# Kernel tuning notes

Measured on AMD Instinct MI355X. Metric: run time of the kernel, lower is better.

Reference implementation:

```python
import jax, jax.numpy as jnp
import numpy as np

N = 100000      # nodes
E = 1200000     # edges
D_IN = 128      # input_dim
H = 64          # hidden_dim
OUT = 3         # output_dim
EPS = 1e-5      # BatchNorm eps


def setup_inputs() -> dict:
    key = jax.random.key(0)
    ks = jax.random.split(key, 24)
    w = lambda k, shape: jax.random.normal(k, shape, jnp.float32) * 0.05
    return {
        "x": jax.random.normal(ks[0], (N, D_IN), jnp.float32),
        "edge_index": jax.random.randint(ks[1], (2, E), 0, N, dtype=jnp.int32),
        "proj_W": w(ks[2], (H, D_IN)), "proj_b": w(ks[3], (H,)),
        "conv1_W": w(ks[4], (H, H)), "conv1_b": w(ks[5], (H,)),
        "bn1_g": jnp.ones((H,), jnp.float32), "bn1_b": w(ks[6], (H,)),
        "conv2_W": w(ks[7], (H, H)), "conv2_b": w(ks[8], (H,)),
        "bn2_g": jnp.ones((H,), jnp.float32), "bn2_b": w(ks[9], (H,)),
        "conv3_W": w(ks[10], (H, H)), "conv3_b": w(ks[11], (H,)),
        "bn3_g": jnp.ones((H,), jnp.float32), "bn3_b": w(ks[12], (H,)),
        "byp_W": w(ks[13], (OUT, D_IN)), "byp_b": w(ks[14], (OUT,)),
        "head_W": w(ks[15], (OUT, H + OUT)), "head_b": w(ks[16], (OUT,)),
    }


def reference(x, edge_index, proj_W, proj_b,
              conv1_W, conv1_b, bn1_g, bn1_b,
              conv2_W, conv2_b, bn2_g, bn2_b,
              conv3_W, conv3_b, bn3_g, bn3_b,
              byp_W, byp_b, head_W, head_b):
    n = x.shape[0]
    row, col = edge_index[0], edge_index[1]
    loop = jnp.arange(n, dtype=row.dtype)
    row_f = jnp.concatenate([row, loop])   # source (with self loops)
    col_f = jnp.concatenate([col, loop])   # target
    # symmetric GCN normalization: deg over targets of A+I, edge weight 1
    deg = jax.ops.segment_sum(jnp.ones(row_f.shape, jnp.float32), col_f, num_segments=n)
    dinv = jnp.where(deg > 0, jax.lax.rsqrt(deg), 0.0)
    norm = dinv[row_f] * dinv[col_f]       # [E+N]

    def gcn(h, W, b):
        h = h @ W.T                                    # transform then propagate
        msg = h[row_f] * norm[:, None]                 # gather + scale
        return jax.ops.segment_sum(msg, col_f, num_segments=n) + b

    def bn(h, g, b):
        # eval-mode BatchNorm1d: running_mean=0, running_var=1 buffers
        return h * (g / jnp.sqrt(1.0 + EPS)) + b

    h = x @ proj_W.T + proj_b
    idn = h
    h = jax.nn.relu(bn(gcn(h, conv1_W, conv1_b), bn1_g, bn1_b)) + idn  # dropout inactive (eval)
    idn = h
    h = jax.nn.relu(bn(gcn(h, conv2_W, conv2_b), bn2_g, bn2_b)) + idn
    h = jax.nn.relu(bn(gcn(h, conv3_W, conv3_b), bn3_g, bn3_b))

    byp = x @ byp_W.T + byp_b
    p = jnp.concatenate([h, byp], axis=1) @ head_W.T + head_b
    kappa = jnp.clip(p[:, 0] * 5.0 + 2.5, 0.2, 10.0)
    alpha = p[:, 1]
    tau = jnp.clip(p[:, 2] + 0.5, 0.05, 2.0)
    return jnp.stack([kappa, alpha, tau], axis=1)
```

## Files before the change

kernel.cpp:

```cpp
#include <hip/hip_runtime.h>
#include <hip/hip_fp16.h>

#define NN 100000
#define NE 1200000
#define NBUK ((NN + 127) / 128)
#define NCHUNK 512
#define NPROJ ((NN + 63) / 64)

typedef _Float16 h8 __attribute__((ext_vector_type(8)));
typedef float f32x4 __attribute__((ext_vector_type(4)));
typedef float f32x2 __attribute__((ext_vector_type(2)));

__global__ __launch_bounds__(256) void k_fusedA(const int* __restrict__ col,
                                                int* __restrict__ blkcnt,
                                                const float* __restrict__ X,
                                                const float* __restrict__ projW,
                                                const float* __restrict__ projb,
                                                const float* __restrict__ bypW,
                                                const float* __restrict__ bypb,
                                                _Float16* __restrict__ Yh,
                                                float* __restrict__ bypOut) {
    constexpr int D = 128, RS = D + 8, KS = D / 32;
    __shared__ _Float16 Xh[64 * RS];
    __shared__ _Float16 Wh[64 * RS];
    const int tid = threadIdx.x;

    if (blockIdx.x < NCHUNK) {
        int* lh = (int*)Xh;
        const int per = (NE + NCHUNK - 1) / NCHUNK;
        const int e0 = blockIdx.x * per;
        const int e1 = (e0 + per < NE) ? (e0 + per) : NE;
        for (int i = tid; i < NBUK; i += 256) lh[i] = 0;
        __syncthreads();
        for (int e = e0 + tid; e < e1; e += 256)
            atomicAdd(&lh[col[e] >> 7], 1);
        __syncthreads();
        for (int b = tid; b < NBUK; b += 256)
            blkcnt[b * NCHUNK + blockIdx.x] = lh[b];
        return;
    }

    const int n0 = (blockIdx.x - NCHUNK) * 64;

    for (int i = tid; i < 64 * (D / 8); i += 256) {
        int j = i / (D / 8), d8 = (i % (D / 8)) * 8;
        const float4* wp = (const float4*)&projW[j * D + d8];
        float4 w0 = wp[0], w1 = wp[1];
        h8 h = { (_Float16)w0.x, (_Float16)w0.y, (_Float16)w0.z, (_Float16)w0.w,
                 (_Float16)w1.x, (_Float16)w1.y, (_Float16)w1.z, (_Float16)w1.w };
        *(h8*)&Wh[j * RS + d8] = h;
    }
    for (int i = tid; i < 64 * (D / 8); i += 256) {
        int nl = i / (D / 8), d8 = (i % (D / 8)) * 8;
        int n = n0 + nl; if (n >= NN) n = NN - 1;
        const float4* xp = (const float4*)&X[(size_t)n * D + d8];
        float4 x0 = xp[0], x1 = xp[1];
        h8 h = { (_Float16)x0.x, (_Float16)x0.y, (_Float16)x0.z, (_Float16)x0.w,
                 (_Float16)x1.x, (_Float16)x1.y, (_Float16)x1.z, (_Float16)x1.w };
        *(h8*)&Xh[nl * RS + d8] = h;
    }
    __syncthreads();

    const int wid = tid >> 6, lane = tid & 63;
    const int lm = lane & 15, lq = lane >> 4;
    const int mBase = wid * 16;

    h8 bfrag[4][KS];
    #pragma unroll
    for (int t = 0; t < 4; ++t)
        #pragma unroll
        for (int s = 0; s < KS; ++s)
            bfrag[t][s] = *(const h8*)&Wh[(t * 16 + lm) * RS + s * 32 + lq * 8];

    h8 bfragB[KS];
    #pragma unroll
    for (int s = 0; s < KS; ++s) {
        if (lm < 3) {
            const float4* wp = (const float4*)&bypW[lm * D + s * 32 + lq * 8];
            float4 w0 = wp[0], w1 = wp[1];
            bfragB[s] = (h8){ (_Float16)w0.x, (_Float16)w0.y, (_Float16)w0.z, (_Float16)w0.w,
                              (_Float16)w1.x, (_Float16)w1.y, (_Float16)w1.z, (_Float16)w1.w };
        } else {
            bfragB[s] = (h8)(_Float16)0;
        }
    }

    f32x4 acc[5] = {};
    #pragma unroll
    for (int s = 0; s < KS; ++s) {
        h8 a = *(const h8*)&Xh[(mBase + lm) * RS + s * 32 + lq * 8];
        #pragma unroll
        for (int t = 0; t < 4; ++t)
            acc[t] = __builtin_amdgcn_mfma_f32_16x16x32_f16(a, bfrag[t][s], acc[t], 0, 0, 0);
        acc[4] = __builtin_amdgcn_mfma_f32_16x16x32_f16(a, bfragB[s], acc[4], 0, 0, 0);
    }

    float bb[4];
    #pragma unroll
    for (int t = 0; t < 4; ++t) bb[t] = projb[t * 16 + lm];
    float bypbv = (lm < 3) ? bypb[lm] : 0.f;
    const int nodeBase = n0 + mBase + lq * 4;

    #pragma unroll
    for (int r = 0; r < 4; ++r) {
        int node = nodeBase + r;
        if (node < NN) {
            #pragma unroll
            for (int t = 0; t < 4; ++t)
                Yh[(size_t)node * 64 + t * 16 + lm] = (_Float16)(acc[t][r] + bb[t]);
            if (lm < 3)
                bypOut[node * 3 + lm] = acc[4][r] + bypbv;
        }
    }
}

__global__ __launch_bounds__(1024) void k_scanAll(int* __restrict__ blkcnt,
                                                  int* __restrict__ bcnt) {
    __shared__ int s[1024];
    const int b = blockIdx.x, tid = threadIdx.x;
    int v = (tid < NCHUNK) ? blkcnt[b * NCHUNK + tid] : 0;
    s[tid] = v;
    __syncthreads();
    #pragma unroll
    for (int d = 1; d < 1024; d <<= 1) {
        int t = (tid >= d) ? s[tid - d] : 0;
        __syncthreads();
        s[tid] += t;
        __syncthreads();
    }
    if (tid < NCHUNK) blkcnt[b * NCHUNK + tid] = s[tid] - v;
    if (tid == 1023) bcnt[b] = s[1023];
}

__global__ __launch_bounds__(256) void k_bucketB(const int* __restrict__ row,
                                                 const int* __restrict__ col,
                                                 const int* __restrict__ bcnt,
                                                 const int* __restrict__ blkcnt,
                                                 unsigned* __restrict__ tmp) {
    __shared__ int lh[NBUK];
    __shared__ int part[256];
    const int tid = threadIdx.x;
    int loc[4]; int sum = 0;
    #pragma unroll
    for (int j = 0; j < 4; ++j) {
        int idx = tid * 4 + j;
        loc[j] = sum;
        sum += (idx < NBUK) ? bcnt[idx] : 0;
    }
    part[tid] = sum;
    __syncthreads();
    #pragma unroll
    for (int d = 1; d < 256; d <<= 1) {
        int t = (tid >= d) ? part[tid - d] : 0;
        __syncthreads();
        part[tid] += t;
        __syncthreads();
    }
    const int excl = part[tid] - sum;
    #pragma unroll
    for (int j = 0; j < 4; ++j) {
        int idx = tid * 4 + j;
        if (idx < NBUK)
            lh[idx] = excl + loc[j] + blkcnt[idx * NCHUNK + blockIdx.x];
    }
    __syncthreads();
    const int per = (NE + NCHUNK - 1) / NCHUNK;
    const int e0 = blockIdx.x * per;
    const int e1 = (e0 + per < NE) ? (e0 + per) : NE;
    for (int e = e0 + tid; e < e1; e += 256) {
        int c = col[e], r = row[e];
        int pos = atomicAdd(&lh[c >> 7], 1);
        tmp[pos] = ((unsigned)r << 7) | (unsigned)(c & 127);
    }
}

__global__ __launch_bounds__(256) void k_buildM(const unsigned* __restrict__ tmp,
                                                const int* __restrict__ bcnt,
                                                int* __restrict__ off,
                                                float* __restrict__ dinv,
                                                int* __restrict__ csr_row,
                                                const _Float16* __restrict__ hA,
                                                const float* __restrict__ W1,
                                                unsigned char* __restrict__ Y8) {
    constexpr int RS2 = 72;
    __shared__ int cnt[128], s[128], cur[128];
    __shared__ int red[256];
    __shared__ float dinvL[128];
    __shared__ _Float16 Hs[128 * RS2];
    __shared__ _Float16 WsL[64 * RS2];
    const int b = blockIdx.x, tid = threadIdx.x;

    for (int i = tid; i < 128 * 8; i += 256) {
        int j = i >> 3, d8 = (i & 7) * 8;
        int n = (b << 7) + j; if (n >= NN) n = NN - 1;
        *(h8*)&Hs[j * RS2 + d8] = *(const h8*)&hA[(size_t)n * 64 + d8];
    }
    for (int i = tid; i < 64 * 8; i += 256) {
        int j = i >> 3, d8 = (i & 7) * 8;
        const float4* wp = (const float4*)&W1[j * 64 + d8];
        float4 w0 = wp[0], w1 = wp[1];
        h8 h = { (_Float16)w0.x, (_Float16)w0.y, (_Float16)w0.z, (_Float16)w0.w,
                 (_Float16)w1.x, (_Float16)w1.y, (_Float16)w1.z, (_Float16)w1.w };
        *(h8*)&WsL[j * RS2 + d8] = h;
    }

    int ssum = 0;
    for (int i = tid; i < b; i += 256) ssum += bcnt[i];
    red[tid] = ssum;
    __syncthreads();
    #pragma unroll
    for (int d = 128; d > 0; d >>= 1) {
        if (tid < d) red[tid] += red[tid + d];
        __syncthreads();
    }
    const int seg0 = red[0];
    const int seg1 = seg0 + bcnt[b];
    const int colBase = b << 7;
    const int nCols = (NN - colBase < 128) ? (NN - colBase) : 128;
    if (tid < 128) cnt[tid] = 0;
    __syncthreads();
    for (int i = seg0 + tid; i < seg1; i += 256)
        atomicAdd(&cnt[tmp[i] & 127], 1);
    __syncthreads();
    if (tid < 128) s[tid] = cnt[tid];
    __syncthreads();
    #pragma unroll
    for (int d = 1; d < 128; d <<= 1) {
        int t = (tid < 128 && tid >= d) ? s[tid - d] : 0;
        __syncthreads();
        if (tid < 128) s[tid] += t;
        __syncthreads();
    }
    if (tid < 128) {
        float dv = rsqrtf((float)cnt[tid] + 1.0f);
        dinvL[tid] = dv;
        if (tid < nCols) {
            int exc = seg0 + s[tid] - cnt[tid];
            off[colBase + tid] = exc;
            cur[tid] = exc;
            dinv[colBase + tid] = dv;
        }
    }
    if (b == 0 && tid == 0) off[NN] = NE;
    __syncthreads();
    for (int i = seg0 + tid; i < seg1; i += 256) {
        unsigned v = tmp[i];
        int pos = atomicAdd(&cur[v & 127u], 1);
        csr_row[pos] = (int)(v >> 7);
    }
    __syncthreads();

    const int wid = tid >> 6, lane = tid & 63;
    const int lm = lane & 15, lq = lane >> 4;
    const int mBase = wid * 16;
    h8 cfrag[4][2];
    #pragma unroll
    for (int t = 0; t < 4; ++t)
        #pragma unroll
        for (int sx = 0; sx < 2; ++sx)
            cfrag[t][sx] = *(const h8*)&WsL[(t * 16 + lm) * RS2 + sx * 32 + lq * 8];
    #pragma unroll
    for (int hh = 0; hh < 2; ++hh) {
        const int rb = hh * 64 + mBase;
        f32x4 acc2[4] = {};
        #pragma unroll
        for (int sx = 0; sx < 2; ++sx) {
            h8 a = *(const h8*)&Hs[(rb + lm) * RS2 + sx * 32 + lq * 8];
            #pragma unroll
            for (int t = 0; t < 4; ++t)
                acc2[t] = __builtin_amdgcn_mfma_f32_16x16x32_f16(a, cfrag[t][sx], acc2[t], 0, 0, 0);
        }
        #pragma unroll
        for (int r = 0; r < 4; ++r) {
            int nl = rb + lq * 4 + r;
            int node = colBase + nl;
            if (node < NN) {
                float sdv = dinvL[nl];
                #pragma unroll
                for (int t = 0; t < 4; ++t) {
                    float v = acc2[t][r] * sdv;
                    int pk = __builtin_amdgcn_cvt_pk_fp8_f32(v, v, 0, false);
                    Y8[(size_t)node * 64 + t * 16 + lm] = (unsigned char)(pk & 0xff);
                }
            }
        }
    }
}

template<bool HEAD>
__global__ __launch_bounds__(256) void k_gather(const unsigned char* __restrict__ hB8,
                                                const float* __restrict__ dinv,
                                                const int* __restrict__ off,
                                                const int* __restrict__ csr_row,
                                                const float* __restrict__ convb,
                                                const float* __restrict__ bng,
                                                const float* __restrict__ bnb,
                                                _Float16* __restrict__ hA,
                                                const float* __restrict__ nextW,
                                                unsigned char* __restrict__ Y8,
                                                const float* __restrict__ byp,
                                                const float* __restrict__ headW,
                                                const float* __restrict__ headb,
                                                float* __restrict__ out) {
    constexpr int RS2 = 72;
    __shared__ _Float16 Ws[HEAD ? 1 : 64 * RS2];
    __shared__ _Float16 Hs[HEAD ? 1 : 32 * RS2];
    __shared__ float HWs[HEAD ? 204 : 1];
    const int tid = threadIdx.x;
    if constexpr (HEAD) {
        for (int i = tid; i < 204; i += 256)
            HWs[i] = (i < 201) ? headW[i] : headb[i - 201];
        __syncthreads();
    } else {
        for (int i = tid; i < 64 * 8; i += 256) {
            int j = i >> 3, d8 = (i & 7) * 8;
            const float4* wp = (const float4*)&nextW[j * 64 + d8];
            float4 w0 = wp[0], w1 = wp[1];
            h8 h = { (_Float16)w0.x, (_Float16)w0.y, (_Float16)w0.z, (_Float16)w0.w,
                     (_Float16)w1.x, (_Float16)w1.y, (_Float16)w1.z, (_Float16)w1.w };
            *(h8*)&Ws[j * RS2 + d8] = h;
        }
    }
    const int wid = tid >> 6, lane = tid & 63;
    const int nloc = wid * 8 + (lane >> 3);
    const int n = blockIdx.x * 32 + nloc;
    const int oct = lane & 7;
    const int f0 = oct * 8;

    const int e0 = off[n];
    const int deg = off[n + 1] - e0;
    int m = deg;
    #pragma unroll
    for (int mask = 8; mask < 64; mask <<= 1) {
        int o = __shfl_xor(m, mask, 64);
        m = (o > m) ? o : m;
    }

    const uint2* rows8 = (const uint2*)hB8;
    float acc[8] = {0, 0, 0, 0, 0, 0, 0, 0};
    uint2 selfw = rows8[(size_t)n * 8 + oct];
    {
        f32x2 p0 = __builtin_amdgcn_cvt_pk_f32_fp8(selfw.x, false);
        f32x2 p1 = __builtin_amdgcn_cvt_pk_f32_fp8(selfw.x, true);
        f32x2 p2 = __builtin_amdgcn_cvt_pk_f32_fp8(selfw.y, false);
        f32x2 p3 = __builtin_amdgcn_cvt_pk_f32_fp8(selfw.y, true);
        acc[0] += p0.x; acc[1] += p0.y; acc[2] += p1.x; acc[3] += p1.y;
        acc[4] += p2.x; acc[5] += p2.y; acc[6] += p3.x; acc[7] += p3.y;
    }
    for (int it = 0; it < m; it += 8) {
        uint2 w[8];
        #pragma unroll
        for (int q = 0; q < 8; ++q) {
            bool vq = it + q < deg;
            int rq = csr_row[vq ? e0 + it + q : 0];
            w[q] = rows8[(size_t)rq * 8 + oct];
            if (!vq) { w[q].x = 0; w[q].y = 0; }
        }
        #pragma unroll
        for (int q = 0; q < 8; ++q) {
            f32x2 p0 = __builtin_amdgcn_cvt_pk_f32_fp8(w[q].x, false);
            f32x2 p1 = __builtin_amdgcn_cvt_pk_f32_fp8(w[q].x, true);
            f32x2 p2 = __builtin_amdgcn_cvt_pk_f32_fp8(w[q].y, false);
            f32x2 p3 = __builtin_amdgcn_cvt_pk_f32_fp8(w[q].y, true);
            acc[0] += p0.x; acc[1] += p0.y; acc[2] += p1.x; acc[3] += p1.y;
            acc[4] += p2.x; acc[5] += p2.y; acc[6] += p3.x; acc[7] += p3.y;
        }
    }

    const float dv = dinv[n];
    const float bnscale = rsqrtf(1.0f + 1e-5f);
    const float4 cb0 = *(const float4*)&convb[f0], cb1 = *(const float4*)&convb[f0 + 4];
    const float4 g0  = *(const float4*)&bng[f0],  g1  = *(const float4*)&bng[f0 + 4];
    const float4 b0_ = *(const float4*)&bnb[f0],  b1_ = *(const float4*)&bnb[f0 + 4];
    const float cb[8] = { cb0.x, cb0.y, cb0.z, cb0.w, cb1.x, cb1.y, cb1.z, cb1.w };
    const float gg[8] = { g0.x, g0.y, g0.z, g0.w, g1.x, g1.y, g1.z, g1.w };
    const float bb[8] = { b0_.x, b0_.y, b0_.z, b0_.w, b1_.x, b1_.y, b1_.z, b1_.w };
    float v[8];
    #pragma unroll
    for (int j = 0; j < 8; ++j)
        v[j] = fmaxf((acc[j] * dv + cb[j]) * (gg[j] * bnscale) + bb[j], 0.0f);

    if constexpr (!HEAD) {
        size_t o = ((size_t)n << 6) + f0;
        h8 old = *(const h8*)&hA[o];
        #pragma unroll
        for (int j = 0; j < 8; ++j) v[j] += (float)old[j];
        h8 res = { (_Float16)v[0], (_Float16)v[1], (_Float16)v[2], (_Float16)v[3],
                   (_Float16)v[4], (_Float16)v[5], (_Float16)v[6], (_Float16)v[7] };
        *(h8*)&hA[o] = res;
        *(h8*)&Hs[nloc * RS2 + f0] = res;
        __syncthreads();

        const int lm = lane & 15, lq = lane >> 4;
        const int mt = (wid & 1) * 16;
        const int nt = (wid >> 1) * 32;
        h8 afrag[2], bfrag[2][2];
        #pragma unroll
        for (int s = 0; s < 2; ++s)
            afrag[s] = *(const h8*)&Hs[(mt + lm) * RS2 + s * 32 + lq * 8];
        #pragma unroll
        for (int t = 0; t < 2; ++t)
            #pragma unroll
            for (int s = 0; s < 2; ++s)
                bfrag[t][s] = *(const h8*)&Ws[(nt + t * 16 + lm) * RS2 + s * 32 + lq * 8];
        f32x4 acc2[2] = {};
        #pragma unroll
        for (int s = 0; s < 2; ++s)
            #pragma unroll
            for (int t = 0; t < 2; ++t)
                acc2[t] = __builtin_amdgcn_mfma_f32_16x16x32_f16(afrag[s], bfrag[t][s], acc2[t], 0, 0, 0);
        const int nodeBase = blockIdx.x * 32 + mt + lq * 4;
        #pragma unroll
        for (int r = 0; r < 4; ++r) {
            int node = nodeBase + r;
            float sdv = dinv[node];
            #pragma unroll
            for (int t = 0; t < 2; ++t) {
                float vv = acc2[t][r] * sdv;
                int pk = __builtin_amdgcn_cvt_pk_fp8_f32(vv, vv, 0, false);
                Y8[(size_t)node * 64 + nt + t * 16 + lm] = (unsigned char)(pk & 0xff);
            }
        }
    } else {
        float p[3];
        #pragma unroll
        for (int o = 0; o < 3; ++o) {
            float t = 0.f;
            #pragma unroll
            for (int j = 0; j < 8; ++j) t += v[j] * HWs[o * 67 + f0 + j];
            p[o] = t;
        }
        #pragma unroll
        for (int mask = 1; mask < 8; mask <<= 1) {
            #pragma unroll
            for (int o = 0; o < 3; ++o) p[o] += __shfl_xor(p[o], mask, 64);
        }
        if (oct == 0) {
            float by0 = byp[n * 3], by1 = byp[n * 3 + 1], by2 = byp[n * 3 + 2];
            #pragma unroll
            for (int o = 0; o < 3; ++o)
                p[o] += by0 * HWs[o * 67 + 64] + by1 * HWs[o * 67 + 65] + by2 * HWs[o * 67 + 66]
                      + HWs[201 + o];
            float kappa = fminf(fmaxf(p[0] * 5.0f + 2.5f, 0.2f), 10.0f);
            float tau   = fminf(fmaxf(p[2] + 0.5f, 0.05f), 2.0f);
            out[(size_t)n * 3]     = kappa;
            out[(size_t)n * 3 + 1] = p[1];
            out[(size_t)n * 3 + 2] = tau;
        }
    }
}

extern "C" void kernel_launch(void* const* d_in, const int* in_sizes, int n_in,
                              void* d_out, int out_size, void* d_ws, size_t ws_size,
                              hipStream_t stream) {
    const float* x     = (const float*)d_in[0];
    const int*   ei    = (const int*)d_in[1];
    const int*   row   = ei;
    const int*   col   = ei + NE;
    const float* projW = (const float*)d_in[2];
    const float* projb = (const float*)d_in[3];
    const float* convW[3] = { (const float*)d_in[4], (const float*)d_in[8],  (const float*)d_in[12] };
    const float* convb[3] = { (const float*)d_in[5], (const float*)d_in[9],  (const float*)d_in[13] };
    const float* bng[3]   = { (const float*)d_in[6], (const float*)d_in[10], (const float*)d_in[14] };
    const float* bnb[3]   = { (const float*)d_in[7], (const float*)d_in[11], (const float*)d_in[15] };
    const float* bypW  = (const float*)d_in[16];
    const float* bypb  = (const float*)d_in[17];
    const float* headW = (const float*)d_in[18];
    const float* headb = (const float*)d_in[19];
    float* out = (float*)d_out;

    float*    ws   = (float*)d_ws;
    float*    dinv = ws;
    _Float16* hAh  = (_Float16*)(ws + 102400);
    unsigned char* hB8a = (unsigned char*)(hAh + (size_t)NN * 64);
    float*    byp  = (float*)(hB8a + (size_t)NN * 64);
    int*      off     = (int*)(byp + 300032);
    int*      csr_row = off + 100096;
    int*      bcnt    = csr_row + NE;
    int*      blkcnt  = bcnt + 784;
    unsigned char* hB8b = (unsigned char*)(blkcnt + (size_t)NBUK * NCHUNK);
    unsigned* tmp     = (unsigned*)(hB8b + (size_t)NN * 64);

    k_fusedA<<<NCHUNK + NPROJ, 256, 0, stream>>>(
        col, blkcnt, x, projW, projb, bypW, bypb, hAh, byp);
    k_scanAll<<<NBUK, 1024, 0, stream>>>(blkcnt, bcnt);
    k_bucketB<<<NCHUNK, 256, 0, stream>>>(row, col, bcnt, blkcnt, tmp);
    k_buildM<<<NBUK, 256, 0, stream>>>(tmp, bcnt, off, dinv, csr_row,
                                       hAh, convW[0], hB8a);

    k_gather<false><<<NN / 32, 256, 0, stream>>>(
        hB8a, dinv, off, csr_row, convb[0], bng[0], bnb[0], hAh,
        convW[1], hB8b, nullptr, nullptr, nullptr, nullptr);
    k_gather<false><<<NN / 32, 256, 0, stream>>>(
        hB8b, dinv, off, csr_row, convb[1], bng[1], bnb[1], hAh,
        convW[2], hB8a, nullptr, nullptr, nullptr, nullptr);
    k_gather<true><<<NN / 32, 256, 0, stream>>>(
        hB8a, dinv, off, csr_row, convb[2], bng[2], bnb[2], nullptr,
        nullptr, nullptr, byp, headW, headb, out);
}
```

Before: 251.8 us.

## Replace two-pass bucket sort CSR build with per-node atomic degree count and scatter

Replaces the chunked bucket-histogram, scan, bucket-scatter and per-bucket local sort with direct global per-node degree atomics, a bucket-sum reduction, per-node offsets computed in k_offM, and a flat atomic scatter of row indices into CSR. This removes the k_scanAll and k_bucketB kernels and the tmp staging buffer. In exchange it issues 1.2M global atomics to the degree array and another 1.2M to the cursor array, which may contend. Edge order within each CSR row also becomes nondeterministic.

```diff
diff --git a/kernel.cpp b/kernel.cpp
--- a/kernel.cpp
+++ b/kernel.cpp
@@ -12,7 +12,8 @@
 typedef float f32x2 __attribute__((ext_vector_type(2)));
 
 __global__ __launch_bounds__(256) void k_fusedA(const int* __restrict__ col,
-                                                int* __restrict__ blkcnt,
+                                                int* __restrict__ deg,
+                                                int* __restrict__ bsum,
                                                 const float* __restrict__ X,
                                                 const float* __restrict__ projW,
                                                 const float* __restrict__ projb,
@@ -32,11 +33,16 @@
         const int e1 = (e0 + per < NE) ? (e0 + per) : NE;
         for (int i = tid; i < NBUK; i += 256) lh[i] = 0;
         __syncthreads();
-        for (int e = e0 + tid; e < e1; e += 256)
-            atomicAdd(&lh[col[e] >> 7], 1);
-        __syncthreads();
-        for (int b = tid; b < NBUK; b += 256)
-            blkcnt[b * NCHUNK + blockIdx.x] = lh[b];
+        for (int e = e0 + tid; e < e1; e += 256) {
+            int c = col[e];
+            atomicAdd(&deg[c], 1);
+            atomicAdd(&lh[c >> 7], 1);
+        }
+        __syncthreads();
+        for (int b = tid; b < NBUK; b += 256) {
+            int v = lh[b];
+            if (v) atomicAdd(&bsum[b], v);
+        }
         return;
     }
 
@@ -114,85 +120,27 @@
     }
 }
 
-__global__ __launch_bounds__(1024) void k_scanAll(int* __restrict__ blkcnt,
-                                                  int* __restrict__ bcnt) {
-    __shared__ int s[1024];
-    const int b = blockIdx.x, tid = threadIdx.x;
-    int v = (tid < NCHUNK) ? blkcnt[b * NCHUNK + tid] : 0;
-    s[tid] = v;
-    __syncthreads();
-    #pragma unroll
-    for (int d = 1; d < 1024; d <<= 1) {
-        int t = (tid >= d) ? s[tid - d] : 0;
-        __syncthreads();
-        s[tid] += t;
-        __syncthreads();
-    }
-    if (tid < NCHUNK) blkcnt[b * NCHUNK + tid] = s[tid] - v;
-    if (tid == 1023) bcnt[b] = s[1023];
-}
-
-__global__ __launch_bounds__(256) void k_bucketB(const int* __restrict__ row,
-                                                 const int* __restrict__ col,
-                                                 const int* __restrict__ bcnt,
-                                                 const int* __restrict__ blkcnt,
-                                                 unsigned* __restrict__ tmp) {
-    __shared__ int lh[NBUK];
-    __shared__ int part[256];
-    const int tid = threadIdx.x;
-    int loc[4]; int sum = 0;
-    #pragma unroll
-    for (int j = 0; j < 4; ++j) {
-        int idx = tid * 4 + j;
-        loc[j] = sum;
-        sum += (idx < NBUK) ? bcnt[idx] : 0;
-    }
-    part[tid] = sum;
-    __syncthreads();
-    #pragma unroll
-    for (int d = 1; d < 256; d <<= 1) {
-        int t = (tid >= d) ? part[tid - d] : 0;
-        __syncthreads();
-        part[tid] += t;
-        __syncthreads();
-    }
-    const int excl = part[tid] - sum;
-    #pragma unroll
-    for (int j = 0; j < 4; ++j) {
-        int idx = tid * 4 + j;
-        if (idx < NBUK)
-            lh[idx] = excl + loc[j] + blkcnt[idx * NCHUNK + blockIdx.x];
-    }
-    __syncthreads();
-    const int per = (NE + NCHUNK - 1) / NCHUNK;
-    const int e0 = blockIdx.x * per;
-    const int e1 = (e0 + per < NE) ? (e0 + per) : NE;
-    for (int e = e0 + tid; e < e1; e += 256) {
-        int c = col[e], r = row[e];
-        int pos = atomicAdd(&lh[c >> 7], 1);
-        tmp[pos] = ((unsigned)r << 7) | (unsigned)(c & 127);
-    }
-}
-
-__global__ __launch_bounds__(256) void k_buildM(const unsigned* __restrict__ tmp,
-                                                const int* __restrict__ bcnt,
-                                                int* __restrict__ off,
-                                                float* __restrict__ dinv,
-                                                int* __restrict__ csr_row,
-                                                const _Float16* __restrict__ hA,
-                                                const float* __restrict__ W1,
-                                                unsigned char* __restrict__ Y8) {
+__global__ __launch_bounds__(256) void k_offM(const int* __restrict__ deg,
+                                              const int* __restrict__ bsum,
+                                              int* __restrict__ off,
+                                              int* __restrict__ cur,
+                                              float* __restrict__ dinv,
+                                              const _Float16* __restrict__ hA,
+                                              const float* __restrict__ W1,
+                                              unsigned char* __restrict__ Y8) {
     constexpr int RS2 = 72;
-    __shared__ int cnt[128], s[128], cur[128];
+    __shared__ int s[128];
     __shared__ int red[256];
     __shared__ float dinvL[128];
     __shared__ _Float16 Hs[128 * RS2];
     __shared__ _Float16 WsL[64 * RS2];
     const int b = blockIdx.x, tid = threadIdx.x;
+    const int colBase = b << 7;
+    const int nCols = (NN - colBase < 128) ? (NN - colBase) : 128;
 
     for (int i = tid; i < 128 * 8; i += 256) {
         int j = i >> 3, d8 = (i & 7) * 8;
-        int n = (b << 7) + j; if (n >= NN) n = NN - 1;
+        int n = colBase + j; if (n >= NN) n = NN - 1;
         *(h8*)&Hs[j * RS2 + d8] = *(const h8*)&hA[(size_t)n * 64 + d8];
     }
     for (int i = tid; i < 64 * 8; i += 256) {
@@ -205,7 +153,7 @@
     }
 
     int ssum = 0;
-    for (int i = tid; i < b; i += 256) ssum += bcnt[i];
+    for (int i = tid; i < b; i += 256) ssum += bsum[i];
     red[tid] = ssum;
     __syncthreads();
     #pragma unroll
@@ -214,15 +162,9 @@
         __syncthreads();
     }
     const int seg0 = red[0];
-    const int seg1 = seg0 + bcnt[b];
-    const int colBase = b << 7;
-    const int nCols = (NN - colBase < 128) ? (NN - colBase) : 128;
-    if (tid < 128) cnt[tid] = 0;
-    __syncthreads();
-    for (int i = seg0 + tid; i < seg1; i += 256)
-        atomicAdd(&cnt[tmp[i] & 127], 1);
-    __syncthreads();
-    if (tid < 128) s[tid] = cnt[tid];
+
+    int dv_ = (tid < nCols) ? deg[colBase + tid] : 0;
+    if (tid < 128) s[tid] = dv_;
     __syncthreads();
     #pragma unroll
     for (int d = 1; d < 128; d <<= 1) {
@@ -232,22 +174,16 @@
         __syncthreads();
     }
     if (tid < 128) {
-        float dv = rsqrtf((float)cnt[tid] + 1.0f);
-        dinvL[tid] = dv;
+        float dvv = rsqrtf((float)dv_ + 1.0f);
+        dinvL[tid] = dvv;
         if (tid < nCols) {
-            int exc = seg0 + s[tid] - cnt[tid];
+            int exc = seg0 + s[tid] - dv_;
             off[colBase + tid] = exc;
-            cur[tid] = exc;
-            dinv[colBase + tid] = dv;
+            cur[colBase + tid] = exc;
+            dinv[colBase + tid] = dvv;
         }
     }
     if (b == 0 && tid == 0) off[NN] = NE;
-    __syncthreads();
-    for (int i = seg0 + tid; i < seg1; i += 256) {
-        unsigned v = tmp[i];
-        int pos = atomicAdd(&cur[v & 127u], 1);
-        csr_row[pos] = (int)(v >> 7);
-    }
     __syncthreads();
 
     const int wid = tid >> 6, lane = tid & 63;
@@ -284,6 +220,19 @@
                 }
             }
         }
+    }
+}
+
+__global__ __launch_bounds__(256) void k_scatter(const int* __restrict__ row,
+                                                 const int* __restrict__ col,
+                                                 int* __restrict__ cur,
+                                                 int* __restrict__ csr_row) {
+    int e = blockIdx.x * 256 + threadIdx.x;
+    const int stride = gridDim.x * 256;
+    for (; e < NE; e += stride) {
+        int c = col[e], r = row[e];
+        int pos = atomicAdd(&cur[c], 1);
+        csr_row[pos] = r;
     }
 }
 
@@ -476,17 +425,18 @@
     float*    byp  = (float*)(hB8a + (size_t)NN * 64);
     int*      off     = (int*)(byp + 300032);
     int*      csr_row = off + 100096;
-    int*      bcnt    = csr_row + NE;
-    int*      blkcnt  = bcnt + 784;
-    unsigned char* hB8b = (unsigned char*)(blkcnt + (size_t)NBUK * NCHUNK);
-    unsigned* tmp     = (unsigned*)(hB8b + (size_t)NN * 64);
+    int*      deg     = csr_row + NE;
+    int*      bsum    = deg + 100096;
+    int*      cur     = bsum + 784;
+    unsigned char* hB8b = (unsigned char*)(cur + 100096);
+
+    hipMemsetAsync(deg, 0, (100096 + 784) * sizeof(int), stream);
 
     k_fusedA<<<NCHUNK + NPROJ, 256, 0, stream>>>(
-        col, blkcnt, x, projW, projb, bypW, bypb, hAh, byp);
-    k_scanAll<<<NBUK, 1024, 0, stream>>>(blkcnt, bcnt);
-    k_bucketB<<<NCHUNK, 256, 0, stream>>>(row, col, bcnt, blkcnt, tmp);
-    k_buildM<<<NBUK, 256, 0, stream>>>(tmp, bcnt, off, dinv, csr_row,
-                                       hAh, convW[0], hB8a);
+        col, deg, bsum, x, projW, projb, bypW, bypb, hAh, byp);
+    k_offM<<<NBUK, 256, 0, stream>>>(deg, bsum, off, cur, dinv,
+                                     hAh, convW[0], hB8a);
+    k_scatter<<<2048, 256, 0, stream>>>(row, col, cur, csr_row);
 
     k_gather<false><<<NN / 32, 256, 0, stream>>>(
         hB8a, dinv, off, csr_row, convb[0], bng[0], bnb[0], hAh,
```

New measurement: 354.6 us. +40.8%, slower.
